# Performance work log

Measured on AMD Instinct MI355X. Metric: run time of the kernel, lower is better.

The kernel has to match this reference:

```python
import jax, jax.numpy as jnp
import numpy as np
from jax import lax

WINDOW_SIZE = 5
SIGMA = 1.0
DILATIONS = [1 + int(i ** 1.5) for i in range(5)]  # [1, 2, 3, 6, 9]
C1 = (0.01 * 255.0) ** 2
C2 = (0.03 * 255.0) ** 2


def _make_window(channel=1):
    x = np.arange(WINDOW_SIZE, dtype=np.float64)
    g = np.exp(-((x - WINDOW_SIZE // 2) ** 2) / (2.0 * SIGMA ** 2))
    g = g / g.sum()
    w2d = np.outer(g, g)
    w2d = w2d / w2d.sum()
    w = np.broadcast_to(w2d[None, None], (channel, 1, WINDOW_SIZE, WINDOW_SIZE))
    return jnp.asarray(w, jnp.float32)


def _dw_conv(x, window, dilation):
    # depthwise 'same' conv; pad = (dilated_kernel - 1)/2 = 2*dilation (always even total pad)
    pad = 2 * dilation
    return lax.conv_general_dilated(
        x, window, window_strides=(1, 1),
        padding=((pad, pad), (pad, pad)),
        rhs_dilation=(dilation, dilation),
        dimension_numbers=('NCHW', 'OIHW', 'NCHW'),
        feature_group_count=window.shape[0])


def _ssim_mean(img1, img2, window, dilation):
    mu1 = _dw_conv(img1, window, dilation)
    mu2 = _dw_conv(img2, window, dilation)
    si11 = _dw_conv(img1 * img1, window, dilation)
    si22 = _dw_conv(img2 * img2, window, dilation)
    si12 = _dw_conv(img1 * img2, window, dilation)
    mu1_sq = mu1 * mu1
    mu2_sq = mu2 * mu2
    mu1_mu2 = mu1 * mu2
    sigma1_sq = si11 - mu1_sq
    sigma2_sq = si22 - mu2_sq
    sigma12 = si12 - mu1_mu2
    ssim_map = ((2.0 * mu1_mu2 + C1) * (2.0 * sigma12 + C2)) / (
        (mu1_sq + mu2_sq + C1) * (sigma1_sq + sigma2_sq + C2))
    return jnp.mean(ssim_map)


def _avg_pool2(x):
    B, C, H, W = x.shape
    return x.reshape(B, C, H // 2, 2, W // 2, 2).mean(axis=(3, 5))


def setup_inputs() -> dict:
    key = jax.random.key(0)
    k1, k2 = jax.random.split(key)
    img1 = jax.random.uniform(k1, (16, 1, 1024, 1024), dtype=jnp.float32)
    img2 = jax.random.uniform(k2, (16, 1, 1024, 1024), dtype=jnp.float32)
    window = _make_window(channel=1)
    weights = jnp.asarray([0.0448, 0.2856, 0.3001, 0.2363, 0.1333], jnp.float32)
    return {"img1": img1, "img2": img2, "window": window, "weights": weights}


def reference(img1, img2, window, weights):
    eps = 1e-12
    m = jnp.max(img2)
    a = (img1 + eps) / (m + eps) * 255.0
    b = (img2 + eps) / (m + eps) * 255.0
    mssim = []
    for dil in DILATIONS:
        mssim.append(_ssim_mean(a, b, window, dil))
        a = _avg_pool2(a)
        b = _avg_pool2(b)
    mssim = jnp.stack(mssim)
    return 1.0 - jnp.prod(mssim ** weights)
```

## Files before the change

kernel.cpp:

```cpp
#include <hip/hip_runtime.h>
#include <math.h>

#define EPSN 1e-12f
#define SSIM_C1 6.5025f
#define SSIM_C2 58.5225f


typedef __attribute__((ext_vector_type(2))) float vf2;
typedef __attribute__((ext_vector_type(2))) _Float16 h2;
typedef __attribute__((ext_vector_type(8))) _Float16 h8;


__global__ void init_ws_kernel(float* ws) {
    if (threadIdx.x < 16) ws[threadIdx.x] = 0.0f;
}


__global__ void max_kernel(const float4* __restrict__ img2, int n4,
                           unsigned* __restrict__ maxbits) {
    float m = 0.0f;
    for (int i = blockIdx.x * blockDim.x + threadIdx.x; i < n4;
         i += gridDim.x * blockDim.x) {
        float4 v = img2[i];
        m = fmaxf(fmaxf(m, fmaxf(v.x, v.y)), fmaxf(v.z, v.w));
    }
#pragma unroll
    for (int o = 32; o > 0; o >>= 1) m = fmaxf(m, __shfl_down(m, o));
    __shared__ float sm[4];
    int tid = threadIdx.x;
    if ((tid & 63) == 0) sm[tid >> 6] = m;
    __syncthreads();
    if (tid == 0) {
        float mm = fmaxf(fmaxf(sm[0], sm[1]), fmaxf(sm[2], sm[3]));
        atomicMax(maxbits, __float_as_uint(mm));
    }
}


__device__ __forceinline__ float ssim_px_h(h2 pm, h2 sq, float s2h) {
    float px = (float)pm.x, py = (float)pm.y;
    float qx = (float)sq.x, qy = (float)sq.y;
    float u = px * px, vv = py * py;
    float upv = u + vv, umv = u - vv;
    float qp = qx + qy, qm = qx - qy;
    float num1 = fmaf(s2h, umv, SSIM_C1);
    float den1 = fmaf(s2h, upv, SSIM_C1);
    float num2 = fmaf(s2h, qm - umv, SSIM_C2);
    float den2 = fmaf(s2h, qp - upv, SSIM_C2);
    return (num1 * num2) * __builtin_amdgcn_rcpf(den1 * den2);
}

__device__ __forceinline__ void load_g1(const float* __restrict__ window,
                                        float* g1) {
#pragma unroll
    for (int k = 0; k < 5; k++)
        g1[k] = ((window[k * 5 + 0] + window[k * 5 + 1]) +
                 (window[k * 5 + 2] + window[k * 5 + 3])) + window[k * 5 + 4];
}

__device__ __forceinline__ void load_g1h(const float* __restrict__ window,
                                         h2* g1h) {
    float g1[5];
    load_g1(window, g1);
#pragma unroll
    for (int k = 0; k < 5; k++)
        g1h[k] = h2{(_Float16)g1[k], (_Float16)g1[k]};
}

__device__ __forceinline__ void block_sum_add(float local, float* part, int tid,
                                              float* __restrict__ sumOut) {
#pragma unroll
    for (int o = 32; o > 0; o >>= 1) local += __shfl_down(local, o);
    if ((tid & 63) == 0) part[tid >> 6] = local;
    __syncthreads();
    if (tid == 0)
        atomicAdd(sumOut, (part[0] + part[1]) + (part[2] + part[3]));
}

template <int D, int TPT, int LW, int L0>
__device__ __forceinline__ float sep_compute(const h2* AB, const h2* g1h,
                                             float s2h, int tx, int ty) {
    h2 rPM[5], rSQ[5];
    float local = 0.0f;
    int rbase = ty * TPT;
#pragma unroll
    for (int ph = 0; ph < D; ++ph) {
        const int cnt = (TPT - ph + D - 1) / D;
#pragma unroll
        for (int k = 0; k < cnt + 4; ++k) {
            const h2* row = AB + (rbase + ph + k * D) * LW + (L0 - 2 * D) + tx;
            h2 hpm = h2{(_Float16)0.f, (_Float16)0.f};
            h2 hsq = h2{(_Float16)0.f, (_Float16)0.f};
#pragma unroll
            for (int kt = 0; kt < 5; kt++) {
                h2 f = row[kt * D];
                h2 w = g1h[kt] * f;
                hpm += w;
                hsq += w * f;
            }
            rPM[k % 5] = hpm;
            rSQ[k % 5] = hsq;
            if (k >= 4) {
                h2 vpm = h2{(_Float16)0.f, (_Float16)0.f};
                h2 vsq = h2{(_Float16)0.f, (_Float16)0.f};
#pragma unroll
                for (int kt = 0; kt < 5; kt++) {
                    int sl = (k - 4 + kt) % 5;
                    vpm += g1h[kt] * rPM[sl];
                    vsq += g1h[kt] * rSQ[sl];
                }
                local += ssim_px_h(vpm, vsq, s2h);
            }
        }
    }
    return local;
}

template <int D, int LH, int LW, int L0, int W>
__device__ __forceinline__ void stage_h2(const h2* __restrict__ base, h2* AB,
                                         int x0i, int y0, int tid) {
    for (int idx = tid; idx < LH * 16; idx += 256) {
        int ly = idx >> 4, j = idx & 15;
        int gy = y0 + ly;
        float4 g = make_float4(0, 0, 0, 0);
        if ((unsigned)gy < (unsigned)W)
            g = *(const float4*)(base + (size_t)gy * W + x0i + 4 * j);
        *(float4*)&AB[ly * LW + L0 + 4 * j] = g;
    }
    for (int idx = tid; idx < LH * 4 * D; idx += 256) {
        int ly = idx / (4 * D), h = idx % (4 * D);
        int gc = (h < 2 * D) ? h : h + 64;
        int gx = x0i - 2 * D + gc, gy = y0 + ly;
        h2 pm = {(_Float16)0.f, (_Float16)0.f};
        if ((unsigned)gx < (unsigned)W && (unsigned)gy < (unsigned)W)
            pm = base[(size_t)gy * W + gx];
        AB[ly * LW + (L0 - 2 * D) + gc] = pm;
    }
}


__global__ __launch_bounds__(256) void ssim0_kernel(
        const float* __restrict__ A, const float* __restrict__ B,
        const float* __restrict__ window, const unsigned* __restrict__ maxbits,
        float* __restrict__ sums, h2* __restrict__ pm1) {
    constexpr int TH = 64, TPT = 16, L0 = 4, LW = 72, LH = 68;
    __shared__ __align__(16) h2 AB[LH * LW];
    __shared__ float part[4];

    int tx = threadIdx.x, ty = threadIdx.y;
    int tid = ty * 64 + tx;
    int b = blockIdx.z;
    int x0i = blockIdx.x * 64;
    int y0 = blockIdx.y * TH - 2;

    const float* Ab = A + (size_t)b * 1024 * 1024;
    const float* Bb = B + (size_t)b * 1024 * 1024;
    for (int idx = tid; idx < LH * 16; idx += 256) {
        int ly = idx >> 4, j = idx & 15;
        int gy = y0 + ly;
        float4 a = make_float4(0, 0, 0, 0), v = make_float4(0, 0, 0, 0);
        if ((unsigned)gy < 1024u) {
            a = *(const float4*)(Ab + (size_t)gy * 1024 + x0i + 4 * j);
            v = *(const float4*)(Bb + (size_t)gy * 1024 + x0i + 4 * j);
        }
        h8 r;
        r[0] = (_Float16)(a.x + v.x); r[1] = (_Float16)(a.x - v.x);
        r[2] = (_Float16)(a.y + v.y); r[3] = (_Float16)(a.y - v.y);
        r[4] = (_Float16)(a.z + v.z); r[5] = (_Float16)(a.z - v.z);
        r[6] = (_Float16)(a.w + v.w); r[7] = (_Float16)(a.w - v.w);
        *(h8*)&AB[ly * LW + L0 + 4 * j] = r;
    }
    for (int idx = tid; idx < LH * 4; idx += 256) {
        int ly = idx >> 2, h = idx & 3;
        int gc = (h < 2) ? h : h + 64;
        int gx = x0i - 2 + gc, gy = y0 + ly;
        h2 pm = {(_Float16)0.f, (_Float16)0.f};
        if ((unsigned)gx < 1024u && (unsigned)gy < 1024u) {
            float a = Ab[(size_t)gy * 1024 + gx], v = Bb[(size_t)gy * 1024 + gx];
            pm = h2{(_Float16)(a + v), (_Float16)(a - v)};
        }
        AB[ly * LW + (L0 - 2) + gc] = pm;
    }
    __syncthreads();

    {
        int py = tid >> 3, j4 = tid & 7;
        const h2* r0 = AB + (2 + 2 * py) * LW + L0 + 8 * j4;
        const h2* r1 = r0 + LW;
        h2 q = {(_Float16)0.25f, (_Float16)0.25f};
        h8 o;
#pragma unroll
        for (int t = 0; t < 4; t++) {
            h2 s = ((r0[2 * t] + r0[2 * t + 1]) + (r1[2 * t] + r1[2 * t + 1])) * q;
            o[2 * t] = s.x; o[2 * t + 1] = s.y;
        }
        int gx = (x0i >> 1) + 4 * j4, gy = blockIdx.y * 32 + py;
        *(h8*)(pm1 + (size_t)b * 512 * 512 + (size_t)gy * 512 + gx) = o;
    }

    h2 g1h[5];
    load_g1h(window, g1h);
    float mx = __uint_as_float(*maxbits);
    float sc = 255.0f / (mx + EPSN);
    float s2h = 0.5f * sc * sc;

    float local = sep_compute<1, TPT, LW, L0>(AB, g1h, s2h, tx, ty);
    block_sum_add(local, part, tid, sums + 0);
}


__global__ __launch_bounds__(256) void ssim1_kernel(
        const h2* __restrict__ pm1, const float* __restrict__ window,
        const unsigned* __restrict__ maxbits, float* __restrict__ sums,
        h2* __restrict__ pm2, h2* __restrict__ pm3, h2* __restrict__ pm4) {
    constexpr int D = 2, TH = 64, TPT = 16, L0 = 4, LW = 72, LH = 72;
    __shared__ __align__(16) h2 AB[LH * LW];
    __shared__ float part[4];

    int tx = threadIdx.x, ty = threadIdx.y;
    int tid = ty * 64 + tx;
    int b = blockIdx.z, bx = blockIdx.x, by = blockIdx.y;
    int x0i = bx * 64, y0 = by * TH - 4;
    const h2* base = pm1 + (size_t)b * 512 * 512;

    stage_h2<D, LH, LW, L0, 512>(base, AB, x0i, y0, tid);
    __syncthreads();

    {
        int py = tid >> 3, j4 = tid & 7;
        const h2* r0 = AB + (4 + 2 * py) * LW + 4 + 8 * j4;
        const h2* r1 = r0 + LW;
        h2 q = {(_Float16)0.25f, (_Float16)0.25f};
        h8 o;
#pragma unroll
        for (int t = 0; t < 4; t++) {
            h2 s = ((r0[2 * t] + r0[2 * t + 1]) + (r1[2 * t] + r1[2 * t + 1])) * q;
            o[2 * t] = s.x; o[2 * t + 1] = s.y;
        }
        int gx = bx * 32 + 4 * j4, gy = by * 32 + py;
        *(h8*)(pm2 + (size_t)b * 256 * 256 + (size_t)gy * 256 + gx) = o;
    }
    {
        int py = tid >> 4, px = tid & 15;
        h2 acc = {(_Float16)0.f, (_Float16)0.f};
#pragma unroll
        for (int ry = 0; ry < 4; ry++)
#pragma unroll
            for (int rx = 0; rx < 4; rx++)
                acc += AB[(4 + 4 * py + ry) * LW + 4 + 4 * px + rx];
        h2 q = {(_Float16)0.0625f, (_Float16)0.0625f};
        acc *= q;
        pm3[(size_t)b * 128 * 128 + (size_t)(by * 16 + py) * 128 + bx * 16 + px] = acc;
    }
    if (tid < 64) {
        int py = tid >> 3, px = tid & 7;
        h2 acc = {(_Float16)0.f, (_Float16)0.f};
#pragma unroll
        for (int ry = 0; ry < 8; ry++)
#pragma unroll
            for (int rx = 0; rx < 8; rx++)
                acc += AB[(4 + 8 * py + ry) * LW + 4 + 8 * px + rx];
        h2 q = {(_Float16)0.015625f, (_Float16)0.015625f};
        acc *= q;
        pm4[(size_t)b * 64 * 64 + (size_t)(by * 8 + py) * 64 + bx * 8 + px] = acc;
    }

    h2 g1h[5];
    load_g1h(window, g1h);
    float mx = __uint_as_float(*maxbits);
    float sc = 255.0f / (mx + EPSN);
    float s2h = 0.5f * sc * sc;

    float local = sep_compute<D, TPT, LW, L0>(AB, g1h, s2h, tx, ty);
    block_sum_add(local, part, tid, sums + 1);
}


template <int D, int TW, int TH, int W, int LW, int LH>
__device__ void direct_level(const h2* __restrict__ base, const h2* g1h,
                             int bx, int by, float s2h, float* part,
                             float* __restrict__ sumOut, h2* AB, int tid) {
    constexpr int NOUT = TW * TH / 256;
    int x0 = bx * TW - 2 * D, y0 = by * TH - 2 * D;

    for (int idx = tid; idx < LW * LH; idx += 256) {
        int ly = idx / LW, lx = idx - ly * LW;
        int px = x0 + lx, py = y0 + ly;
        h2 pm = {(_Float16)0.f, (_Float16)0.f};
        if ((unsigned)px < (unsigned)W && (unsigned)py < (unsigned)W)
            pm = base[(size_t)py * W + px];
        AB[idx] = pm;
    }
    __syncthreads();

    h2 mu[NOUT], sq[NOUT];
#pragma unroll
    for (int j = 0; j < NOUT; j++) {
        mu[j] = h2{(_Float16)0.f, (_Float16)0.f};
        sq[j] = h2{(_Float16)0.f, (_Float16)0.f};
    }
#pragma unroll
    for (int ky = 0; ky < 5; ky++) {
#pragma unroll
        for (int kx = 0; kx < 5; kx++) {
            h2 wh = g1h[ky] * g1h[kx];
#pragma unroll
            for (int j = 0; j < NOUT; j++) {
                int lin = tid + j * 256;
                int ox = lin % TW, oy = lin / TW;
                h2 f = AB[(oy + ky * D) * LW + ox + kx * D];
                h2 wf = wh * f;
                mu[j] += wf;
                sq[j] += wf * f;
            }
        }
    }
    float local = 0.0f;
#pragma unroll
    for (int j = 0; j < NOUT; j++) local += ssim_px_h(mu[j], sq[j], s2h);
    block_sum_add(local, part, tid, sumOut);
}

__global__ __launch_bounds__(256) void tail_kernel(
        const h2* __restrict__ pm2, const h2* __restrict__ pm3,
        const h2* __restrict__ pm4, const float* __restrict__ window,
        const unsigned* __restrict__ maxbits, float* __restrict__ sums,
        unsigned* __restrict__ counter, const float* __restrict__ weights,
        unsigned* __restrict__ out) {
    extern __shared__ __align__(16) h2 ldsdyn[];
    __shared__ float part[4];
    int tid = threadIdx.x;

    h2 g1h[5];
    load_g1h(window, g1h);
    float mx = __uint_as_float(*maxbits);
    float sc = 255.0f / (mx + EPSN);
    float s2h = 0.5f * sc * sc;

    int bid = blockIdx.x;
    if (bid < 512) {
        int b = bid >> 5, r = bid & 31, by = r >> 2, bx = r & 3;
        constexpr int D = 3, TPT = 8, L0 = 8, LW = 80, LH = 44;
        const h2* base = pm2 + (size_t)b * 256 * 256;
        stage_h2<D, LH, LW, L0, 256>(base, ldsdyn, bx * 64, by * 32 - 6, tid);
        __syncthreads();
        float local = sep_compute<D, TPT, LW, L0>(ldsdyn, g1h, s2h,
                                                  tid & 63, tid >> 6);
        block_sum_add(local, part, tid, sums + 2);
    } else if (bid < 768) {
        int t = bid - 512, b = t >> 4, r = t & 15, by = r >> 1, bx = r & 1;
        const h2* base = pm3 + (size_t)b * 128 * 128;
        direct_level<6, 64, 16, 128, 88, 40>(base, g1h, bx, by, s2h, part,
                                             sums + 3, ldsdyn, tid);
    } else {
        int t = bid - 768, b = t >> 3, r = t & 7, by = r >> 1, bx = r & 1;
        const h2* base = pm4 + (size_t)b * 64 * 64;
        direct_level<9, 32, 16, 64, 68, 52>(base, g1h, bx, by, s2h, part,
                                            sums + 4, ldsdyn, tid);
    }

    if (tid == 0) {
        __threadfence();
        if (atomicAdd(counter, 1u) == 895u) {
            __threadfence();
            const float counts[5] = {16.0f * 1024 * 1024, 16.0f * 512 * 512,
                                     16.0f * 256 * 256,   16.0f * 128 * 128,
                                     16.0f * 64 * 64};
            float prod = 1.0f;
#pragma unroll
            for (int i = 0; i < 5; i++) {
                float m = atomicAdd(sums + i, 0.0f) / counts[i];
                prod *= powf(m, weights[i]);
            }
            float r = 1.0f - prod;
            unsigned bits = __float_as_uint(r);
            unsigned lsb = (bits >> 16) & 1u;
            unsigned hi = (bits + 0x7FFFu + lsb) >> 16;
            out[0] = (hi << 16) | hi;
        }
    }
}


extern "C" void kernel_launch(void* const* d_in, const int* in_sizes, int n_in,
                              void* d_out, int out_size, void* d_ws, size_t ws_size,
                              hipStream_t stream) {
    const float* img1 = (const float*)d_in[0];
    const float* img2 = (const float*)d_in[1];
    const float* window = (const float*)d_in[2];
    const float* weights = (const float*)d_in[3];

    float* ws = (float*)d_ws;
    unsigned* maxbits = (unsigned*)d_ws;
    float* sums = ws + 4;
    unsigned* counter = (unsigned*)(ws + 10);
    size_t off = 512;
    h2* pm1 = (h2*)(ws + off); off += (size_t)16 * 512 * 512;
    h2* pm2 = (h2*)(ws + off); off += (size_t)16 * 256 * 256;
    h2* pm3 = (h2*)(ws + off); off += (size_t)16 * 128 * 128;
    h2* pm4 = (h2*)(ws + off); off += (size_t)16 * 64 * 64;

    init_ws_kernel<<<1, 64, 0, stream>>>(ws);
    max_kernel<<<2048, 256, 0, stream>>>((const float4*)img2,
                                         16 * 1024 * 1024 / 4, maxbits);
    ssim0_kernel<<<dim3(16, 16, 16), dim3(64, 4), 0, stream>>>(
        img1, img2, window, maxbits, sums, pm1);
    ssim1_kernel<<<dim3(8, 8, 16), dim3(64, 4), 0, stream>>>(
        pm1, window, maxbits, sums, pm2, pm3, pm4);
    tail_kernel<<<896, 256, 14144, stream>>>(pm2, pm3, pm4, window, maxbits,
                                             sums, counter, weights,
                                             (unsigned*)d_out);
}
```

Measured before the change: 277.5 us.

## Shrink ssim0 tiles to 128 threads, batch global loads, prefetch LDS rows

The level-0 SSIM kernel moves from 64x64 tiles with 256 threads to 64x32 tiles with 128 threads and a narrower LDS row pitch. All global loads are now issued into registers before any conversion, so more memory requests are in flight at once. The separable convolution loop prefetches the next row's five taps from LDS into registers one iteration ahead. The smaller tile raises the share of halo rows that are reloaded, and the register batching adds register pressure in exchange for more blocks and better latency hiding.

```diff
diff --git a/kernel.cpp b/kernel.cpp
--- a/kernel.cpp
+++ b/kernel.cpp
@@ -8,6 +8,7 @@
 
 typedef __attribute__((ext_vector_type(2))) float vf2;
 typedef __attribute__((ext_vector_type(2))) _Float16 h2;
+typedef __attribute__((ext_vector_type(4))) _Float16 h4;
 typedef __attribute__((ext_vector_type(8))) _Float16 h8;
 
 
@@ -50,21 +51,14 @@
     return (num1 * num2) * __builtin_amdgcn_rcpf(den1 * den2);
 }
 
-__device__ __forceinline__ void load_g1(const float* __restrict__ window,
-                                        float* g1) {
-#pragma unroll
-    for (int k = 0; k < 5; k++)
-        g1[k] = ((window[k * 5 + 0] + window[k * 5 + 1]) +
-                 (window[k * 5 + 2] + window[k * 5 + 3])) + window[k * 5 + 4];
-}
-
 __device__ __forceinline__ void load_g1h(const float* __restrict__ window,
                                          h2* g1h) {
-    float g1[5];
-    load_g1(window, g1);
-#pragma unroll
-    for (int k = 0; k < 5; k++)
-        g1h[k] = h2{(_Float16)g1[k], (_Float16)g1[k]};
+#pragma unroll
+    for (int k = 0; k < 5; k++) {
+        float g = ((window[k * 5 + 0] + window[k * 5 + 1]) +
+                   (window[k * 5 + 2] + window[k * 5 + 3])) + window[k * 5 + 4];
+        g1h[k] = h2{(_Float16)g, (_Float16)g};
+    }
 }
 
 __device__ __forceinline__ void block_sum_add(float local, float* part, int tid,
@@ -75,6 +69,15 @@
     __syncthreads();
     if (tid == 0)
         atomicAdd(sumOut, (part[0] + part[1]) + (part[2] + part[3]));
+}
+
+__device__ __forceinline__ void block_sum_add2(float local, float* part, int tid,
+                                               float* __restrict__ sumOut) {
+#pragma unroll
+    for (int o = 32; o > 0; o >>= 1) local += __shfl_down(local, o);
+    if ((tid & 63) == 0) part[tid >> 6] = local;
+    __syncthreads();
+    if (tid == 0) atomicAdd(sumOut, part[0] + part[1]);
 }
 
 template <int D, int TPT, int LW, int L0>
@@ -86,17 +89,27 @@
 #pragma unroll
     for (int ph = 0; ph < D; ++ph) {
         const int cnt = (TPT - ph + D - 1) / D;
+        const h2* col = AB + (rbase + ph) * LW + (L0 - 2 * D) + tx;
+        h2 fN[5];
+#pragma unroll
+        for (int kt = 0; kt < 5; kt++) fN[kt] = col[kt * D];
 #pragma unroll
         for (int k = 0; k < cnt + 4; ++k) {
-            const h2* row = AB + (rbase + ph + k * D) * LW + (L0 - 2 * D) + tx;
+            h2 f[5];
+#pragma unroll
+            for (int kt = 0; kt < 5; kt++) f[kt] = fN[kt];
+            if (k + 1 < cnt + 4) {
+                const h2* row = col + (k + 1) * D * LW;
+#pragma unroll
+                for (int kt = 0; kt < 5; kt++) fN[kt] = row[kt * D];
+            }
             h2 hpm = h2{(_Float16)0.f, (_Float16)0.f};
             h2 hsq = h2{(_Float16)0.f, (_Float16)0.f};
 #pragma unroll
             for (int kt = 0; kt < 5; kt++) {
-                h2 f = row[kt * D];
-                h2 w = g1h[kt] * f;
+                h2 w = g1h[kt] * f[kt];
                 hpm += w;
-                hsq += w * f;
+                hsq += w * f[kt];
             }
             rPM[k % 5] = hpm;
             rSQ[k % 5] = hsq;
@@ -125,7 +138,14 @@
         float4 g = make_float4(0, 0, 0, 0);
         if ((unsigned)gy < (unsigned)W)
             g = *(const float4*)(base + (size_t)gy * W + x0i + 4 * j);
-        *(float4*)&AB[ly * LW + L0 + 4 * j] = g;
+        h2* p = &AB[ly * LW + L0 + 4 * j];
+        if constexpr ((L0 & 3) == 2) {
+            h8 r = __builtin_bit_cast(h8, g);
+            *(h4*)p = h4{r[0], r[1], r[2], r[3]};
+            *(h4*)(p + 2) = h4{r[4], r[5], r[6], r[7]};
+        } else {
+            *(float4*)p = g;
+        }
     }
     for (int idx = tid; idx < LH * 4 * D; idx += 256) {
         int ly = idx / (4 * D), h = idx % (4 * D);
@@ -139,47 +159,65 @@
 }
 
 
-__global__ __launch_bounds__(256) void ssim0_kernel(
+__global__ __launch_bounds__(128) void ssim0_kernel(
         const float* __restrict__ A, const float* __restrict__ B,
         const float* __restrict__ window, const unsigned* __restrict__ maxbits,
         float* __restrict__ sums, h2* __restrict__ pm1) {
-    constexpr int TH = 64, TPT = 16, L0 = 4, LW = 72, LH = 68;
+    constexpr int TPT = 16, L0 = 2, LW = 68, LH = 36;
     __shared__ __align__(16) h2 AB[LH * LW];
-    __shared__ float part[4];
-
-    int tx = threadIdx.x, ty = threadIdx.y;
-    int tid = ty * 64 + tx;
+    __shared__ float part[2];
+
+    int tid = threadIdx.y * 64 + threadIdx.x;
     int b = blockIdx.z;
     int x0i = blockIdx.x * 64;
-    int y0 = blockIdx.y * TH - 2;
+    int y0 = blockIdx.y * 32 - 2;
 
     const float* Ab = A + (size_t)b * 1024 * 1024;
     const float* Bb = B + (size_t)b * 1024 * 1024;
-    for (int idx = tid; idx < LH * 16; idx += 256) {
-        int ly = idx >> 4, j = idx & 15;
+
+    float4 a[5], v[5];
+#pragma unroll
+    for (int j = 0; j < 5; j++) {
+        int idx = tid + 128 * j;
+        int ly = idx >> 4, c = idx & 15;
         int gy = y0 + ly;
-        float4 a = make_float4(0, 0, 0, 0), v = make_float4(0, 0, 0, 0);
-        if ((unsigned)gy < 1024u) {
-            a = *(const float4*)(Ab + (size_t)gy * 1024 + x0i + 4 * j);
-            v = *(const float4*)(Bb + (size_t)gy * 1024 + x0i + 4 * j);
-        }
-        h8 r;
-        r[0] = (_Float16)(a.x + v.x); r[1] = (_Float16)(a.x - v.x);
-        r[2] = (_Float16)(a.y + v.y); r[3] = (_Float16)(a.y - v.y);
-        r[4] = (_Float16)(a.z + v.z); r[5] = (_Float16)(a.z - v.z);
-        r[6] = (_Float16)(a.w + v.w); r[7] = (_Float16)(a.w - v.w);
-        *(h8*)&AB[ly * LW + L0 + 4 * j] = r;
-    }
-    for (int idx = tid; idx < LH * 4; idx += 256) {
-        int ly = idx >> 2, h = idx & 3;
-        int gc = (h < 2) ? h : h + 64;
-        int gx = x0i - 2 + gc, gy = y0 + ly;
-        h2 pm = {(_Float16)0.f, (_Float16)0.f};
-        if ((unsigned)gx < 1024u && (unsigned)gy < 1024u) {
-            float a = Ab[(size_t)gy * 1024 + gx], v = Bb[(size_t)gy * 1024 + gx];
-            pm = h2{(_Float16)(a + v), (_Float16)(a - v)};
-        }
-        AB[ly * LW + (L0 - 2) + gc] = pm;
+        a[j] = make_float4(0, 0, 0, 0);
+        v[j] = make_float4(0, 0, 0, 0);
+        if (idx < LH * 16 && (unsigned)gy < 1024u) {
+            a[j] = *(const float4*)(Ab + (size_t)gy * 1024 + x0i + 4 * c);
+            v[j] = *(const float4*)(Bb + (size_t)gy * 1024 + x0i + 4 * c);
+        }
+    }
+#pragma unroll
+    for (int j = 0; j < 5; j++) {
+        int idx = tid + 128 * j;
+        if (idx < LH * 16) {
+            int ly = idx >> 4, c = idx & 15;
+            h8 r;
+            r[0] = (_Float16)(a[j].x + v[j].x); r[1] = (_Float16)(a[j].x - v[j].x);
+            r[2] = (_Float16)(a[j].y + v[j].y); r[3] = (_Float16)(a[j].y - v[j].y);
+            r[4] = (_Float16)(a[j].z + v[j].z); r[5] = (_Float16)(a[j].z - v[j].z);
+            r[6] = (_Float16)(a[j].w + v[j].w); r[7] = (_Float16)(a[j].w - v[j].w);
+            h2* p = &AB[ly * LW + L0 + 4 * c];
+            *(h4*)p = h4{r[0], r[1], r[2], r[3]};
+            *(h4*)(p + 2) = h4{r[4], r[5], r[6], r[7]};
+        }
+    }
+#pragma unroll
+    for (int j = 0; j < 2; j++) {
+        int idx = tid + 128 * j;
+        if (idx < LH * 4) {
+            int ly = idx >> 2, h = idx & 3;
+            int gc = (h < 2) ? h : h + 64;
+            int gx = x0i - 2 + gc, gy = y0 + ly;
+            h2 pm = {(_Float16)0.f, (_Float16)0.f};
+            if ((unsigned)gx < 1024u && (unsigned)gy < 1024u) {
+                float aa = Ab[(size_t)gy * 1024 + gx];
+                float vv = Bb[(size_t)gy * 1024 + gx];
+                pm = h2{(_Float16)(aa + vv), (_Float16)(aa - vv)};
+            }
+            AB[ly * LW + (L0 - 2) + gc] = pm;
+        }
     }
     __syncthreads();
 
@@ -194,7 +232,7 @@
             h2 s = ((r0[2 * t] + r0[2 * t + 1]) + (r1[2 * t] + r1[2 * t + 1])) * q;
             o[2 * t] = s.x; o[2 * t + 1] = s.y;
         }
-        int gx = (x0i >> 1) + 4 * j4, gy = blockIdx.y * 32 + py;
+        int gx = (x0i >> 1) + 4 * j4, gy = blockIdx.y * 16 + py;
         *(h8*)(pm1 + (size_t)b * 512 * 512 + (size_t)gy * 512 + gx) = o;
     }
 
@@ -204,8 +242,8 @@
     float sc = 255.0f / (mx + EPSN);
     float s2h = 0.5f * sc * sc;
 
-    float local = sep_compute<1, TPT, LW, L0>(AB, g1h, s2h, tx, ty);
-    block_sum_add(local, part, tid, sums + 0);
+    float local = sep_compute<1, TPT, LW, L0>(AB, g1h, s2h, tid & 63, tid >> 6);
+    block_sum_add2(local, part, tid, sums + 0);
 }
 
 
@@ -403,7 +441,7 @@
     init_ws_kernel<<<1, 64, 0, stream>>>(ws);
     max_kernel<<<2048, 256, 0, stream>>>((const float4*)img2,
                                          16 * 1024 * 1024 / 4, maxbits);
-    ssim0_kernel<<<dim3(16, 16, 16), dim3(64, 4), 0, stream>>>(
+    ssim0_kernel<<<dim3(16, 32, 16), dim3(64, 2), 0, stream>>>(
         img1, img2, window, maxbits, sums, pm1);
     ssim1_kernel<<<dim3(8, 8, 16), dim3(64, 4), 0, stream>>>(
         pm1, window, maxbits, sums, pm2, pm3, pm4);
```

Measured after the change: 323.2 us. 1.16x slower.
